# Performance work log

Hardware: AMD Instinct MI355X
Metric: run time of the kernel (lower is better)

## Reference

```python
import jax, jax.numpy as jnp
import numpy as np
import math

B, T, D = 2, 1024, 128
H, DH = 64, 2
SCALE = math.sqrt(DH)
TEMPERATURE = 0.8

def setup_inputs() -> dict:
    key = jax.random.key(0)
    ks = jax.random.split(key, 5)
    inv = 1.0 / math.sqrt(D)
    return {
        "x": jax.random.normal(ks[0], (B, T, D), dtype=jnp.float32),
        "Wq": jax.random.normal(ks[1], (D, D), dtype=jnp.float32) * inv,
        "Wk": jax.random.normal(ks[2], (D, D), dtype=jnp.float32) * inv,
        "Wv": jax.random.normal(ks[3], (D, D), dtype=jnp.float32) * inv,
        "Wo": jax.random.normal(ks[4], (D, D), dtype=jnp.float32) * inv,
    }

def reference(x, Wq, Wk, Wv, Wo):
    b, t, d = x.shape
    # torch nn.Linear(bias=False): y = x @ W.T
    Q = (x @ Wq.T).reshape(b, t, H, DH).transpose(0, 2, 1, 3)  # (B,H,T,dh)
    K = (x @ Wk.T).reshape(b, t, H, DH).transpose(0, 2, 1, 3)
    V = (x @ Wv.T).reshape(b, t, H, DH).transpose(0, 2, 1, 3)
    # scores / sqrt(d_head) / temperature, causal mask (strict upper -> -inf)
    scores = jnp.einsum("bhqd,bhkd->bhqk", Q, K) / (SCALE * TEMPERATURE)
    causal = jnp.triu(jnp.ones((t, t), dtype=bool), k=1)  # True above diagonal
    scores = jnp.where(causal, -jnp.inf, scores)
    attn = jax.nn.softmax(scores, axis=-1)  # dropout is identity in eval mode
    out = jnp.einsum("bhqk,bhkd->bhqd", attn, V)
    out = out.transpose(0, 2, 1, 3).reshape(b, t, d)
    return out @ Wo.T
```

## Files before the change

kernel.cpp:

```cpp
#include <hip/hip_runtime.h>
#include <math.h>

#define Tdim 1024
#define Hh   64

__device__ __constant__ float kQScale = 0.8838834764831844f * 1.4426950408889634f;

__global__ __launch_bounds__(256) void qkv_proj(
    const float* __restrict__ x, const float* __restrict__ Wq,
    const float* __restrict__ Wk, const float* __restrict__ Wv,
    float* __restrict__ Q, float* __restrict__ KV)
{
    __shared__ float xs[16][128];
    __shared__ float Wch[128][36];

    const int tid  = threadIdx.x;
    const int row0 = blockIdx.x * 16;
    const int w    = blockIdx.y;

    {
        const float4* xg = reinterpret_cast<const float4*>(x + (size_t)row0 * 128);
        reinterpret_cast<float4*>(&xs[0][0])[tid]       = xg[tid];
        reinterpret_cast<float4*>(&xs[0][0])[tid + 256] = xg[tid + 256];
    }

    const float* W = (w == 0) ? Wq : (w == 1) ? Wk : Wv;

    const int j0 = tid & 31;
    const int r0 = (tid >> 5) << 1;

    float acc[2][4];
#pragma unroll
    for (int r = 0; r < 2; ++r)
#pragma unroll
        for (int c = 0; c < 4; ++c) acc[r][c] = 0.f;

    for (int ch = 0; ch < 4; ++ch) {
        __syncthreads();
#pragma unroll
        for (int s = 0; s < 4; ++s) {
            const int idx  = tid + s * 256;
            const int rowW = idx >> 3;
            const int c4   = idx & 7;
            *reinterpret_cast<float4*>(&Wch[rowW][c4 * 4]) =
                reinterpret_cast<const float4*>(W + (size_t)rowW * 128 + ch * 32)[c4];
        }
        __syncthreads();

#pragma unroll
        for (int c = 0; c < 8; ++c) {
            const float4 w0 = *reinterpret_cast<const float4*>(&Wch[j0      ][c * 4]);
            const float4 w1 = *reinterpret_cast<const float4*>(&Wch[j0 + 32 ][c * 4]);
            const float4 w2 = *reinterpret_cast<const float4*>(&Wch[j0 + 64 ][c * 4]);
            const float4 w3 = *reinterpret_cast<const float4*>(&Wch[j0 + 96 ][c * 4]);
#pragma unroll
            for (int r = 0; r < 2; ++r) {
                const float4 xv = *reinterpret_cast<const float4*>(&xs[r0 + r][ch * 32 + c * 4]);
                acc[r][0] = fmaf(xv.x, w0.x, fmaf(xv.y, w0.y, fmaf(xv.z, w0.z, fmaf(xv.w, w0.w, acc[r][0]))));
                acc[r][1] = fmaf(xv.x, w1.x, fmaf(xv.y, w1.y, fmaf(xv.z, w1.z, fmaf(xv.w, w1.w, acc[r][1]))));
                acc[r][2] = fmaf(xv.x, w2.x, fmaf(xv.y, w2.y, fmaf(xv.z, w2.z, fmaf(xv.w, w2.w, acc[r][2]))));
                acc[r][3] = fmaf(xv.x, w3.x, fmaf(xv.y, w3.y, fmaf(xv.z, w3.z, fmaf(xv.w, w3.w, acc[r][3]))));
            }
        }
    }

#pragma unroll
    for (int r = 0; r < 2; ++r) {
        const int row = row0 + r0 + r;
        const int bb  = row >> 10;
        const int t   = row & 1023;
#pragma unroll
        for (int jj = 0; jj < 4; ++jj) {
            const int j = j0 + jj * 32;
            const float v = acc[r][jj];
            if (w == 0) {
                Q[(size_t)row * 128 + j] = v * kQScale;
            } else {
                const int h  = j >> 1, dh = j & 1;
                const int bh = bb * Hh + h;
                KV[((size_t)bh * Tdim + t) * 4 + ((w == 1) ? dh : 2 + dh)] = v;
            }
        }
    }
}

__global__ __launch_bounds__(256) void attn(
    const float* __restrict__ Q, const float4* __restrict__ KV,
    float* __restrict__ O)
{
    __shared__ float4 KVs[Tdim];
    const int tid   = threadIdx.x;
    const int chunk = blockIdx.x;
    const int bh    = blockIdx.y;
    const int nk    = chunk * 64 + 64;

    const float4* KVg = KV + (size_t)bh * Tdim;
    for (int i = tid; i < nk; i += 256) KVs[i] = KVg[i];
    __syncthreads();

    const int t   = chunk * 64 + (tid >> 2);
    const int sub = tid & 3;
    const int b   = bh >> 6, h = bh & 63;
    const float2 q = *reinterpret_cast<const float2*>(
        Q + (size_t)(b * Tdim + t) * 128 + h * 2);

    float l = 0.f, a0 = 0.f, a1 = 0.f;
#pragma unroll 4
    for (int k = sub; k <= t; k += 4) {
        const float4 kv = KVs[k];
        const float p = exp2f(fmaf(q.x, kv.x, q.y * kv.y));
        l  += p;
        a0 = fmaf(p, kv.z, a0);
        a1 = fmaf(p, kv.w, a1);
    }

    l  += __shfl_xor(l, 1);  l  += __shfl_xor(l, 2);
    a0 += __shfl_xor(a0, 1); a0 += __shfl_xor(a0, 2);
    a1 += __shfl_xor(a1, 1); a1 += __shfl_xor(a1, 2);

    if (sub == 0) {
        const float rl = 1.0f / l;
        float* Op = O + (size_t)(b * Tdim + t) * 128 + h * 2;
        Op[0] = a0 * rl;
        Op[1] = a1 * rl;
    }
}

__global__ __launch_bounds__(256) void out_proj(
    const float* __restrict__ Oin, const float* __restrict__ Wo,
    float* __restrict__ out)
{
    __shared__ float xs[16][128];
    __shared__ float Wch[128][36];

    const int tid  = threadIdx.x;
    const int row0 = blockIdx.x * 16;

    {
        const float4* xg = reinterpret_cast<const float4*>(Oin + (size_t)row0 * 128);
        reinterpret_cast<float4*>(&xs[0][0])[tid]       = xg[tid];
        reinterpret_cast<float4*>(&xs[0][0])[tid + 256] = xg[tid + 256];
    }

    const int j0 = tid & 31;
    const int r0 = (tid >> 5) << 1;

    float acc[2][4];
#pragma unroll
    for (int r = 0; r < 2; ++r)
#pragma unroll
        for (int c = 0; c < 4; ++c) acc[r][c] = 0.f;

    for (int ch = 0; ch < 4; ++ch) {
        __syncthreads();
#pragma unroll
        for (int s = 0; s < 4; ++s) {
            const int idx  = tid + s * 256;
            const int rowW = idx >> 3;
            const int c4   = idx & 7;
            *reinterpret_cast<float4*>(&Wch[rowW][c4 * 4]) =
                reinterpret_cast<const float4*>(Wo + (size_t)rowW * 128 + ch * 32)[c4];
        }
        __syncthreads();

#pragma unroll
        for (int c = 0; c < 8; ++c) {
            const float4 w0 = *reinterpret_cast<const float4*>(&Wch[j0      ][c * 4]);
            const float4 w1 = *reinterpret_cast<const float4*>(&Wch[j0 + 32 ][c * 4]);
            const float4 w2 = *reinterpret_cast<const float4*>(&Wch[j0 + 64 ][c * 4]);
            const float4 w3 = *reinterpret_cast<const float4*>(&Wch[j0 + 96 ][c * 4]);
#pragma unroll
            for (int r = 0; r < 2; ++r) {
                const float4 xv = *reinterpret_cast<const float4*>(&xs[r0 + r][ch * 32 + c * 4]);
                acc[r][0] = fmaf(xv.x, w0.x, fmaf(xv.y, w0.y, fmaf(xv.z, w0.z, fmaf(xv.w, w0.w, acc[r][0]))));
                acc[r][1] = fmaf(xv.x, w1.x, fmaf(xv.y, w1.y, fmaf(xv.z, w1.z, fmaf(xv.w, w1.w, acc[r][1]))));
                acc[r][2] = fmaf(xv.x, w2.x, fmaf(xv.y, w2.y, fmaf(xv.z, w2.z, fmaf(xv.w, w2.w, acc[r][2]))));
                acc[r][3] = fmaf(xv.x, w3.x, fmaf(xv.y, w3.y, fmaf(xv.z, w3.z, fmaf(xv.w, w3.w, acc[r][3]))));
            }
        }
    }

#pragma unroll
    for (int r = 0; r < 2; ++r) {
        const int row = row0 + r0 + r;
#pragma unroll
        for (int jj = 0; jj < 4; ++jj) {
            const int j = j0 + jj * 32;
            out[(size_t)row * 128 + j] = acc[r][jj];
        }
    }
}

extern "C" void kernel_launch(void* const* d_in, const int* in_sizes, int n_in,
                              void* d_out, int out_size, void* d_ws, size_t ws_size,
                              hipStream_t stream) {
    const float* x  = (const float*)d_in[0];
    const float* Wq = (const float*)d_in[1];
    const float* Wk = (const float*)d_in[2];
    const float* Wv = (const float*)d_in[3];
    const float* Wo = (const float*)d_in[4];
    float* out = (float*)d_out;

    float* ws = (float*)d_ws;
    float* Q  = ws;
    float* KV = ws + 262144;
    float* O  = ws + 786432;

    qkv_proj<<<dim3(128, 3), 256, 0, stream>>>(x, Wq, Wk, Wv, Q, KV);
    attn<<<dim3(16, 128), 256, 0, stream>>>(Q, (const float4*)KV, O);
    out_proj<<<128, 256, 0, stream>>>(O, Wo, out);
}
```

Measured before the change: 117.3 us.

## Pair low and high causal query chunks per block, four queries per thread

The attention kernel now pairs query chunk c with chunk 15-c in one block, so every block does the same amount of causal work. Each thread handles four queries (two rows from each chunk) and eight lanes split the keys, so each shared-memory KV load feeds several exp/FMA updates. The grid is halved and the raw amdgcn exp2 builtin replaces exp2f. In exchange there are more registers per thread, more complex boundary handling, fewer blocks, and possibly reduced exp2 precision.

```diff
diff --git a/kernel.cpp b/kernel.cpp
--- a/kernel.cpp
+++ b/kernel.cpp
@@ -3,6 +3,12 @@
 
 #define Tdim 1024
 #define Hh   64
+
+#if __has_builtin(__builtin_amdgcn_exp2f)
+#define EXP2(x) __builtin_amdgcn_exp2f(x)
+#else
+#define EXP2(x) exp2f(x)
+#endif
 
 __device__ __constant__ float kQScale = 0.8838834764831844f * 1.4426950408889634f;
 
@@ -90,39 +96,78 @@
 {
     __shared__ float4 KVs[Tdim];
     const int tid   = threadIdx.x;
-    const int chunk = blockIdx.x;
+    const int c     = blockIdx.x;
     const int bh    = blockIdx.y;
-    const int nk    = chunk * 64 + 64;
+    const int lowb  = c * 64;
+    const int highb = (15 - c) * 64;
+    const int nk    = highb + 64;
 
     const float4* KVg = KV + (size_t)bh * Tdim;
     for (int i = tid; i < nk; i += 256) KVs[i] = KVg[i];
     __syncthreads();
 
-    const int t   = chunk * 64 + (tid >> 2);
-    const int sub = tid & 3;
+    const int sub = tid & 7;
+    const int g   = tid >> 3;
+    const int lq  = lowb + g * 2;
+    const int hq  = highb + g * 2;
     const int b   = bh >> 6, h = bh & 63;
-    const float2 q = *reinterpret_cast<const float2*>(
-        Q + (size_t)(b * Tdim + t) * 128 + h * 2);
-
-    float l = 0.f, a0 = 0.f, a1 = 0.f;
+
+    const float* Qb = Q + (size_t)b * (Tdim * 128) + h * 2;
+    float2 q[4];
+    q[0] = *reinterpret_cast<const float2*>(Qb + (size_t)(lq    ) * 128);
+    q[1] = *reinterpret_cast<const float2*>(Qb + (size_t)(lq + 1) * 128);
+    q[2] = *reinterpret_cast<const float2*>(Qb + (size_t)(hq    ) * 128);
+    q[3] = *reinterpret_cast<const float2*>(Qb + (size_t)(hq + 1) * 128);
+
+    float l[4]  = {0.f, 0.f, 0.f, 0.f};
+    float a0[4] = {0.f, 0.f, 0.f, 0.f};
+    float a1[4] = {0.f, 0.f, 0.f, 0.f};
+
+    auto upd = [&](int i, const float4 kv) {
+        const float p = EXP2(fmaf(q[i].x, kv.x, q[i].y * kv.y));
+        l[i] += p;
+        a0[i] = fmaf(p, kv.z, a0[i]);
+        a1[i] = fmaf(p, kv.w, a1[i]);
+    };
+
+#pragma unroll 2
+    for (int k = sub; k < lq; k += 8) {
+        const float4 kv = KVs[k];
+        upd(0, kv); upd(1, kv); upd(2, kv); upd(3, kv);
+    }
+    if (sub <= 1) {
+        const float4 kv = KVs[lq + sub];
+        if (sub == 0) upd(0, kv);
+        upd(1, kv);
+    }
+    int k2 = (lq & ~7) + sub; if (k2 < lq) k2 += 8;
 #pragma unroll 4
-    for (int k = sub; k <= t; k += 4) {
+    for (int k = k2; k < hq; k += 8) {
         const float4 kv = KVs[k];
-        const float p = exp2f(fmaf(q.x, kv.x, q.y * kv.y));
-        l  += p;
-        a0 = fmaf(p, kv.z, a0);
-        a1 = fmaf(p, kv.w, a1);
-    }
-
-    l  += __shfl_xor(l, 1);  l  += __shfl_xor(l, 2);
-    a0 += __shfl_xor(a0, 1); a0 += __shfl_xor(a0, 2);
-    a1 += __shfl_xor(a1, 1); a1 += __shfl_xor(a1, 2);
+        upd(2, kv); upd(3, kv);
+    }
+    if (sub <= 1) {
+        const float4 kv = KVs[hq + sub];
+        if (sub == 0) upd(2, kv);
+        upd(3, kv);
+    }
+
+#pragma unroll
+    for (int i = 0; i < 4; ++i) {
+        l[i]  += __shfl_xor(l[i], 1);  l[i]  += __shfl_xor(l[i], 2);  l[i]  += __shfl_xor(l[i], 4);
+        a0[i] += __shfl_xor(a0[i], 1); a0[i] += __shfl_xor(a0[i], 2); a0[i] += __shfl_xor(a0[i], 4);
+        a1[i] += __shfl_xor(a1[i], 1); a1[i] += __shfl_xor(a1[i], 2); a1[i] += __shfl_xor(a1[i], 4);
+    }
 
     if (sub == 0) {
-        const float rl = 1.0f / l;
-        float* Op = O + (size_t)(b * Tdim + t) * 128 + h * 2;
-        Op[0] = a0 * rl;
-        Op[1] = a1 * rl;
+        float* Ob = O + (size_t)b * (Tdim * 128) + h * 2;
+#pragma unroll
+        for (int i = 0; i < 4; ++i) {
+            const int row = (i < 2) ? (lq + i) : (hq + i - 2);
+            const float rl = 1.0f / l[i];
+            *reinterpret_cast<float2*>(Ob + (size_t)row * 128) =
+                make_float2(a0[i] * rl, a1[i] * rl);
+        }
     }
 }
 
@@ -207,6 +252,6 @@
     float* O  = ws + 786432;
 
     qkv_proj<<<dim3(128, 3), 256, 0, stream>>>(x, Wq, Wk, Wv, Q, KV);
-    attn<<<dim3(16, 128), 256, 0, stream>>>(Q, (const float4*)KV, O);
+    attn<<<dim3(8, 128), 256, 0, stream>>>(Q, (const float4*)KV, O);
     out_proj<<<128, 256, 0, stream>>>(O, Wo, out);
 }
```

Result: faster. 95.34 us (-18.7%).
